# Optimization experiments

Measured on AMD Instinct MI355X. Metric: run time of the kernel, lower is better.

The kernel has to match this reference:

```python
import jax, jax.numpy as jnp
import numpy as np

B, IN, OUT, ZD = 128, 1024, 1024, 128
A_MIN = 0.2


def setup_inputs() -> dict:
    key = jax.random.key(0)
    ks = jax.random.split(key, 8)
    x = jax.random.normal(ks[0], (B, IN), dtype=jnp.float32)
    z = jax.random.normal(ks[1], (B, ZD), dtype=jnp.float32)
    base_weight = jax.random.normal(ks[2], (OUT, IN), dtype=jnp.float32) * (2.0 / IN) ** 0.5
    # nn.Linear(z_dim, out*in): weight [out*in, z_dim], bias [out*in]
    lim_w = 1.0 / np.sqrt(ZD)
    dw_W = jax.random.uniform(ks[3], (OUT * IN, ZD), minval=-lim_w, maxval=lim_w, dtype=jnp.float32)
    dw_b = jax.random.uniform(ks[4], (OUT * IN,), minval=-lim_w, maxval=lim_w, dtype=jnp.float32)
    base_bias = jnp.zeros((OUT,), dtype=jnp.float32)
    db_W = jax.random.uniform(ks[5], (OUT, ZD), minval=-lim_w, maxval=lim_w, dtype=jnp.float32)
    db_b = jax.random.uniform(ks[6], (OUT,), minval=-lim_w, maxval=lim_w, dtype=jnp.float32)
    s = jnp.asarray(2.0, dtype=jnp.float32)
    return {"x": x, "z": z, "base_weight": base_weight, "dw_W": dw_W, "dw_b": dw_b,
            "base_bias": base_bias, "db_W": db_W, "db_b": db_b, "s": s}


def reference(x, z, base_weight, dw_W, dw_b, base_bias, db_W, db_b, s):
    # eval mode: a = a_min * sigmoid(s)
    a = A_MIN * jax.nn.sigmoid(s)
    # hypernetwork head: delta_w = Linear(z) -> [B, OUT, IN]
    delta_w = (jnp.einsum('bz,oz->bo', z, dw_W) + dw_b).reshape(x.shape[0], OUT, IN)
    # per-sample blended weight
    w = a * base_weight[None, :, :] + (1.0 - a) * delta_w  # [B, OUT, IN]
    # batched matvec
    out = jnp.einsum('boi,bi->bo', w, x)
    # blended bias
    delta_b = jnp.einsum('bz,oz->bo', z, db_W) + db_b  # [B, OUT]
    b = a * base_bias + (1.0 - a) * delta_b
    return out + b
```

## Files before the change

kernel.cpp:

```cpp
#include <hip/hip_runtime.h>
#include <cmath>

#define Bsz   128
#define INsz  1024
#define OUTsz 1024
#define ZDsz  128

typedef __bf16 bf16x8 __attribute__((ext_vector_type(8)));
typedef float  floatx4 __attribute__((ext_vector_type(4)));

__global__ __launch_bounds__(256, 2) void hyper_fused_kernel(
    const float* __restrict__ x, const float* __restrict__ z,
    const float* __restrict__ W, const float* __restrict__ dwW,
    const float* __restrict__ dwb, const float* __restrict__ bb,
    const float* __restrict__ dbW, const float* __restrict__ dbb,
    const float* __restrict__ s, float* __restrict__ out)
{
    __shared__ __align__(16) __bf16 zt[128 * 136];
    __shared__ float oacc[16 * 128];

    int t    = threadIdx.x;
    int lane = t & 63;
    int wave = t >> 6;
    int quad = lane >> 4;
    int l15  = lane & 15;

    float a     = 0.2f / (1.f + __expf(-s[0]));
    float one_a = 1.f - a;
    float ratio = a / one_a;

    {
        int b = t >> 1;
        int half = (t & 1) * 64;
        const float4* zrow = reinterpret_cast<const float4*>(z + (size_t)b * ZDsz + half);
        __bf16* dst = &zt[b * 136 + half];
        #pragma unroll
        for (int j = 0; j < 16; ++j) {
            float4 v = zrow[j];
            dst[j*4+0] = (__bf16)v.x; dst[j*4+1] = (__bf16)v.y;
            dst[j*4+2] = (__bf16)v.z; dst[j*4+3] = (__bf16)v.w;
        }
    }
    #pragma unroll
    for (int j = 0; j < 8; ++j) oacc[t * 8 + j] = 0.f;
    __syncthreads();

    bf16x8 bfrag[8][4];
    #pragma unroll
    for (int sj = 0; sj < 8; ++sj)
        #pragma unroll
        for (int k = 0; k < 4; ++k)
            bfrag[sj][k] = *reinterpret_cast<const bf16x8*>(
                &zt[(sj * 16 + l15) * 136 + k * 32 + quad * 8]);

    int otile = blockIdx.x * 16;
    int ibase = blockIdx.y * 128;

    for (int it = 0; it < 8; ++it) {
        int i0 = ibase + it * 16;
        #pragma unroll 1
        for (int c = 0; c < 4; ++c) {
            int o = otile + wave * 4 + c;

            float4 Wv = *reinterpret_cast<const float4*>(W   + (size_t)o * INsz + i0 + quad * 4);
            float4 Dv = *reinterpret_cast<const float4*>(dwb + (size_t)o * INsz + i0 + quad * 4);

            const float* abase = dwW + ((size_t)o * INsz + i0 + l15) * ZDsz + quad * 8;
            bf16x8 afrag[4];
            #pragma unroll
            for (int k = 0; k < 4; ++k) {
                float4 lo = *reinterpret_cast<const float4*>(abase + k * 32);
                float4 hi = *reinterpret_cast<const float4*>(abase + k * 32 + 4);
                afrag[k][0]=(__bf16)lo.x; afrag[k][1]=(__bf16)lo.y;
                afrag[k][2]=(__bf16)lo.z; afrag[k][3]=(__bf16)lo.w;
                afrag[k][4]=(__bf16)hi.x; afrag[k][5]=(__bf16)hi.y;
                afrag[k][6]=(__bf16)hi.z; afrag[k][7]=(__bf16)hi.w;
            }

            float wex0 = Dv.x + ratio * Wv.x;
            float wex1 = Dv.y + ratio * Wv.y;
            float wex2 = Dv.z + ratio * Wv.z;
            float wex3 = Dv.w + ratio * Wv.w;

            #pragma unroll
            for (int sj = 0; sj < 8; ++sj) {
                floatx4 cf = {0.f, 0.f, 0.f, 0.f};
                #pragma unroll
                for (int k = 0; k < 4; ++k)
                    cf = __builtin_amdgcn_mfma_f32_16x16x32_bf16(afrag[k], bfrag[sj][k], cf, 0, 0, 0);
                const floatx4 xv = *reinterpret_cast<const floatx4*>(
                    x + (size_t)(sj * 16 + l15) * INsz + i0 + quad * 4);
                float p = (cf[0] + wex0) * xv[0] + (cf[1] + wex1) * xv[1]
                        + (cf[2] + wex2) * xv[2] + (cf[3] + wex3) * xv[3];
                p += __shfl_xor(p, 16);
                p += __shfl_xor(p, 32);
                if (lane < 16) oacc[(wave * 4 + c) * 128 + sj * 16 + l15] += p;
            }
        }
    }

    if (blockIdx.y == 0) {
        __syncthreads();
        const float* abase = dbW + (size_t)(otile + l15) * ZDsz + quad * 8;
        bf16x8 afrag[4];
        #pragma unroll
        for (int k = 0; k < 4; ++k) {
            float4 lo = *reinterpret_cast<const float4*>(abase + k * 32);
            float4 hi = *reinterpret_cast<const float4*>(abase + k * 32 + 4);
            afrag[k][0]=(__bf16)lo.x; afrag[k][1]=(__bf16)lo.y;
            afrag[k][2]=(__bf16)lo.z; afrag[k][3]=(__bf16)lo.w;
            afrag[k][4]=(__bf16)hi.x; afrag[k][5]=(__bf16)hi.y;
            afrag[k][6]=(__bf16)hi.z; afrag[k][7]=(__bf16)hi.w;
        }
        float4 bbv  = *reinterpret_cast<const float4*>(bb  + otile + quad * 4);
        float4 dbbv = *reinterpret_cast<const float4*>(dbb + otile + quad * 4);
        float bias0 = ratio * bbv.x + dbbv.x, bias1 = ratio * bbv.y + dbbv.y;
        float bias2 = ratio * bbv.z + dbbv.z, bias3 = ratio * bbv.w + dbbv.w;
        #pragma unroll
        for (int u = 0; u < 2; ++u) {
            int sj = wave * 2 + u;
            floatx4 cf = {0.f, 0.f, 0.f, 0.f};
            #pragma unroll
            for (int k = 0; k < 4; ++k)
                cf = __builtin_amdgcn_mfma_f32_16x16x32_bf16(afrag[k], bfrag[sj][k], cf, 0, 0, 0);
            oacc[(quad * 4 + 0) * 128 + sj * 16 + l15] += cf[0] + bias0;
            oacc[(quad * 4 + 1) * 128 + sj * 16 + l15] += cf[1] + bias1;
            oacc[(quad * 4 + 2) * 128 + sj * 16 + l15] += cf[2] + bias2;
            oacc[(quad * 4 + 3) * 128 + sj * 16 + l15] += cf[3] + bias3;
        }
    }
    __syncthreads();

    {
        int b = t >> 1;
        int og = (t & 1) * 8;
        #pragma unroll
        for (int j = 0; j < 8; ++j)
            atomicAdd(&out[(size_t)b * OUTsz + otile + og + j],
                      one_a * oacc[(og + j) * 128 + b]);
    }
}

extern "C" void kernel_launch(void* const* d_in, const int* in_sizes, int n_in,
                              void* d_out, int out_size, void* d_ws, size_t ws_size,
                              hipStream_t stream) {
    (void)in_sizes; (void)n_in; (void)d_ws; (void)ws_size;
    const float* x   = (const float*)d_in[0];
    const float* z   = (const float*)d_in[1];
    const float* W   = (const float*)d_in[2];
    const float* dwW = (const float*)d_in[3];
    const float* dwb = (const float*)d_in[4];
    const float* bb  = (const float*)d_in[5];
    const float* dbW = (const float*)d_in[6];
    const float* dbb = (const float*)d_in[7];
    const float* s   = (const float*)d_in[8];
    float* out = (float*)d_out;

    hipMemsetAsync(out, 0, (size_t)out_size * sizeof(float), stream);
    hyper_fused_kernel<<<dim3(OUTsz / 16, 8), 256, 0, stream>>>(
        x, z, W, dwW, dwb, bb, dbW, dbb, s, out);
}
```

Before: 737.4 us.

## Prefetch next dwW tile into registers and stage x slice in LDS as bf16

Flattens the (it, c) loops into one loop of 32 iterations. The fp32 dwW fragment, W and dwb for the next iteration are loaded into registers while the MFMAs for the current one run, which is meant to hide HBM latency on the dominant 512MB dwW stream. The block's x slice is cached in shared memory as bf16, reusing the z buffer after the B fragments are in registers, instead of re-reading x from global memory every iteration. In exchange it adds register pressure (32 extra floats of prefetch) that may hurt occupancy, and it lowers x precision to bf16.

```diff
diff --git a/kernel.cpp b/kernel.cpp
--- a/kernel.cpp
+++ b/kernel.cpp
@@ -7,6 +7,7 @@
 #define ZDsz  128
 
 typedef __bf16 bf16x8 __attribute__((ext_vector_type(8)));
+typedef __bf16 bf16x4 __attribute__((ext_vector_type(4)));
 typedef float  floatx4 __attribute__((ext_vector_type(4)));
 
 __global__ __launch_bounds__(256, 2) void hyper_fused_kernel(
@@ -16,7 +17,7 @@
     const float* __restrict__ dbW, const float* __restrict__ dbb,
     const float* __restrict__ s, float* __restrict__ out)
 {
-    __shared__ __align__(16) __bf16 zt[128 * 136];
+    __shared__ __align__(16) __bf16 smem[128 * 136];
     __shared__ float oacc[16 * 128];
 
     int t    = threadIdx.x;
@@ -24,22 +25,23 @@
     int wave = t >> 6;
     int quad = lane >> 4;
     int l15  = lane & 15;
+    int l31  = lane & 31;
+    int rowp = lane >> 5;
 
     float a     = 0.2f / (1.f + __expf(-s[0]));
     float one_a = 1.f - a;
     float ratio = a / one_a;
 
-    {
-        int b = t >> 1;
-        int half = (t & 1) * 64;
-        const float4* zrow = reinterpret_cast<const float4*>(z + (size_t)b * ZDsz + half);
-        __bf16* dst = &zt[b * 136 + half];
-        #pragma unroll
-        for (int j = 0; j < 16; ++j) {
-            float4 v = zrow[j];
-            dst[j*4+0] = (__bf16)v.x; dst[j*4+1] = (__bf16)v.y;
-            dst[j*4+2] = (__bf16)v.z; dst[j*4+3] = (__bf16)v.w;
-        }
+    int otile = blockIdx.x * 16;
+    int ibase = blockIdx.y * 128;
+
+    #pragma unroll
+    for (int j = 0; j < 16; ++j) {
+        int r  = wave * 32 + 2 * j + rowp;
+        int cc = l31 * 4;
+        float4 v = *reinterpret_cast<const float4*>(z + (size_t)r * ZDsz + cc);
+        __bf16* d = &smem[r * 136 + cc];
+        d[0] = (__bf16)v.x; d[1] = (__bf16)v.y; d[2] = (__bf16)v.z; d[3] = (__bf16)v.w;
     }
     #pragma unroll
     for (int j = 0; j < 8; ++j) oacc[t * 8 + j] = 0.f;
@@ -51,62 +53,78 @@
         #pragma unroll
         for (int k = 0; k < 4; ++k)
             bfrag[sj][k] = *reinterpret_cast<const bf16x8*>(
-                &zt[(sj * 16 + l15) * 136 + k * 32 + quad * 8]);
+                &smem[(sj * 16 + l15) * 136 + k * 32 + quad * 8]);
+    __syncthreads();
 
-    int otile = blockIdx.x * 16;
-    int ibase = blockIdx.y * 128;
+    #pragma unroll
+    for (int j = 0; j < 16; ++j) {
+        int r  = wave * 32 + 2 * j + rowp;
+        int cc = l31 * 4;
+        float4 v = *reinterpret_cast<const float4*>(x + (size_t)r * INsz + ibase + cc);
+        __bf16* d = &smem[r * 136 + cc];
+        d[0] = (__bf16)v.x; d[1] = (__bf16)v.y; d[2] = (__bf16)v.z; d[3] = (__bf16)v.w;
+    }
+    __syncthreads();
 
-    for (int it = 0; it < 8; ++it) {
+    float4 avlo[4], avhi[4], Wv, Dv;
+    auto load_iter = [&](int idx) {
+        int it = idx >> 2, c = idx & 3;
         int i0 = ibase + it * 16;
-        #pragma unroll 1
-        for (int c = 0; c < 4; ++c) {
-            int o = otile + wave * 4 + c;
+        int o  = otile + wave * 4 + c;
+        const float* ab = dwW + ((size_t)o * INsz + i0 + l15) * ZDsz + quad * 8;
+        #pragma unroll
+        for (int k = 0; k < 4; ++k) {
+            avlo[k] = *reinterpret_cast<const float4*>(ab + k * 32);
+            avhi[k] = *reinterpret_cast<const float4*>(ab + k * 32 + 4);
+        }
+        Wv = *reinterpret_cast<const float4*>(W   + (size_t)o * INsz + i0 + quad * 4);
+        Dv = *reinterpret_cast<const float4*>(dwb + (size_t)o * INsz + i0 + quad * 4);
+    };
+    load_iter(0);
 
-            float4 Wv = *reinterpret_cast<const float4*>(W   + (size_t)o * INsz + i0 + quad * 4);
-            float4 Dv = *reinterpret_cast<const float4*>(dwb + (size_t)o * INsz + i0 + quad * 4);
+    #pragma unroll 1
+    for (int idx = 0; idx < 32; ++idx) {
+        int it = idx >> 2, c = idx & 3;
 
-            const float* abase = dwW + ((size_t)o * INsz + i0 + l15) * ZDsz + quad * 8;
-            bf16x8 afrag[4];
+        bf16x8 afrag[4];
+        #pragma unroll
+        for (int k = 0; k < 4; ++k) {
+            afrag[k][0]=(__bf16)avlo[k].x; afrag[k][1]=(__bf16)avlo[k].y;
+            afrag[k][2]=(__bf16)avlo[k].z; afrag[k][3]=(__bf16)avlo[k].w;
+            afrag[k][4]=(__bf16)avhi[k].x; afrag[k][5]=(__bf16)avhi[k].y;
+            afrag[k][6]=(__bf16)avhi[k].z; afrag[k][7]=(__bf16)avhi[k].w;
+        }
+        float wex0 = Dv.x + ratio * Wv.x;
+        float wex1 = Dv.y + ratio * Wv.y;
+        float wex2 = Dv.z + ratio * Wv.z;
+        float wex3 = Dv.w + ratio * Wv.w;
+
+        if (idx < 31) load_iter(idx + 1);
+
+        #pragma unroll
+        for (int sj = 0; sj < 8; ++sj) {
+            floatx4 cf = {0.f, 0.f, 0.f, 0.f};
             #pragma unroll
-            for (int k = 0; k < 4; ++k) {
-                float4 lo = *reinterpret_cast<const float4*>(abase + k * 32);
-                float4 hi = *reinterpret_cast<const float4*>(abase + k * 32 + 4);
-                afrag[k][0]=(__bf16)lo.x; afrag[k][1]=(__bf16)lo.y;
-                afrag[k][2]=(__bf16)lo.z; afrag[k][3]=(__bf16)lo.w;
-                afrag[k][4]=(__bf16)hi.x; afrag[k][5]=(__bf16)hi.y;
-                afrag[k][6]=(__bf16)hi.z; afrag[k][7]=(__bf16)hi.w;
-            }
-
-            float wex0 = Dv.x + ratio * Wv.x;
-            float wex1 = Dv.y + ratio * Wv.y;
-            float wex2 = Dv.z + ratio * Wv.z;
-            float wex3 = Dv.w + ratio * Wv.w;
-
-            #pragma unroll
-            for (int sj = 0; sj < 8; ++sj) {
-                floatx4 cf = {0.f, 0.f, 0.f, 0.f};
-                #pragma unroll
-                for (int k = 0; k < 4; ++k)
-                    cf = __builtin_amdgcn_mfma_f32_16x16x32_bf16(afrag[k], bfrag[sj][k], cf, 0, 0, 0);
-                const floatx4 xv = *reinterpret_cast<const floatx4*>(
-                    x + (size_t)(sj * 16 + l15) * INsz + i0 + quad * 4);
-                float p = (cf[0] + wex0) * xv[0] + (cf[1] + wex1) * xv[1]
-                        + (cf[2] + wex2) * xv[2] + (cf[3] + wex3) * xv[3];
-                p += __shfl_xor(p, 16);
-                p += __shfl_xor(p, 32);
-                if (lane < 16) oacc[(wave * 4 + c) * 128 + sj * 16 + l15] += p;
-            }
+            for (int k = 0; k < 4; ++k)
+                cf = __builtin_amdgcn_mfma_f32_16x16x32_bf16(afrag[k], bfrag[sj][k], cf, 0, 0, 0);
+            bf16x4 xr = *reinterpret_cast<const bf16x4*>(
+                &smem[(sj * 16 + l15) * 136 + it * 16 + quad * 4]);
+            float p = (cf[0] + wex0) * (float)xr[0] + (cf[1] + wex1) * (float)xr[1]
+                    + (cf[2] + wex2) * (float)xr[2] + (cf[3] + wex3) * (float)xr[3];
+            p += __shfl_xor(p, 16);
+            p += __shfl_xor(p, 32);
+            if (lane < 16) oacc[(wave * 4 + c) * 128 + sj * 16 + l15] += p;
         }
     }
 
     if (blockIdx.y == 0) {
         __syncthreads();
-        const float* abase = dbW + (size_t)(otile + l15) * ZDsz + quad * 8;
+        const float* ab = dbW + (size_t)(otile + l15) * ZDsz + quad * 8;
         bf16x8 afrag[4];
         #pragma unroll
         for (int k = 0; k < 4; ++k) {
-            float4 lo = *reinterpret_cast<const float4*>(abase + k * 32);
-            float4 hi = *reinterpret_cast<const float4*>(abase + k * 32 + 4);
+            float4 lo = *reinterpret_cast<const float4*>(ab + k * 32);
+            float4 hi = *reinterpret_cast<const float4*>(ab + k * 32 + 4);
             afrag[k][0]=(__bf16)lo.x; afrag[k][1]=(__bf16)lo.y;
             afrag[k][2]=(__bf16)lo.z; afrag[k][3]=(__bf16)lo.w;
             afrag[k][4]=(__bf16)hi.x; afrag[k][5]=(__bf16)hi.y;
@@ -132,7 +150,7 @@
     __syncthreads();
 
     {
-        int b = t >> 1;
+        int b  = t >> 1;
         int og = (t & 1) * 8;
         #pragma unroll
         for (int j = 0; j < 8; ++j)
```

Result: no change. 730.5 us (-0.9%).
